# Performance work log

Measured on AMD Instinct MI355X. Metric: run time of the kernel, lower is better.

The kernel has to match this reference:

```python
import jax, jax.numpy as jnp
import numpy as np

N_NODES = 50000
N_EDGES = 300000
D = 256
EPS = 1e-12


def setup_inputs() -> dict:
    key = jax.random.key(0)
    ks = jax.random.split(key, 10)
    h5_all = jax.random.normal(ks[0], (N_NODES, D), dtype=jnp.float32)
    edge_index = jax.random.randint(ks[1], (2, N_EDGES), 0, N_NODES, dtype=jnp.int64)
    edge_weight = jax.random.uniform(ks[2], (N_EDGES,), dtype=jnp.float32)
    s = 1.0 / np.sqrt(D)
    W6 = jax.random.normal(ks[3], (D, D), dtype=jnp.float32) * s
    b6 = jnp.zeros((D,), dtype=jnp.float32)
    W7 = jax.random.normal(ks[4], (D, D), dtype=jnp.float32) * s
    b7 = jnp.zeros((D,), dtype=jnp.float32)
    Wp = jax.random.normal(ks[5], (D, D), dtype=jnp.float32) * s
    bp = jnp.zeros((D,), dtype=jnp.float32)
    return {"h5_all": h5_all, "edge_index": edge_index, "edge_weight": edge_weight,
            "W6": W6, "b6": b6, "W7": W7, "b7": b7, "Wp": Wp, "bp": bp}


def _gcn_layer(x, W, b, src, dst, norm, n_nodes):
    # x: [N, D]; transform then gather-scale-scatter along edges
    xt = x @ W                                   # [N, D]
    msg = xt[src] * norm[:, None]                # [E, D] gathered + scaled
    agg = jax.ops.segment_sum(msg, dst, num_segments=n_nodes)  # [N, D]
    return jax.nn.relu(agg + b)


def reference(h5_all, edge_index, edge_weight, W6, b6, W7, b7, Wp, bp):
    src, dst = edge_index[0], edge_index[1]
    # symmetric degree normalization with edge weights (GCN-style)
    deg_out = jax.ops.segment_sum(edge_weight, src, num_segments=N_NODES)
    deg_in = jax.ops.segment_sum(edge_weight, dst, num_segments=N_NODES)
    norm = edge_weight * jax.lax.rsqrt(deg_out[src] * deg_in[dst] + EPS)  # [E]
    h6 = _gcn_layer(h5_all, W6, b6, src, dst, norm, N_NODES)
    h7 = _gcn_layer(h6, W7, b7, src, dst, norm, N_NODES)
    out = h7 @ Wp + bp                           # post_mp linear head
    return out
```

## Files before the change

### kernel.cpp

```cpp
#include <hip/hip_runtime.h>

#define N_NODES 50000
#define N_PAD   50048
#define N_PANELS 3125
#define N_EDGES 300000
#define EPS_F 1e-12f
#define EB ((N_EDGES + 255) / 256)
#define GB 512
#define SCAN_NB ((N_NODES + 255) / 256)
#define MASK48 ((1ull << 48) - 1)
#define ZBYTES (N_NODES * 20)

typedef _Float16 f16x8 __attribute__((ext_vector_type(8)));
typedef float f32x4 __attribute__((ext_vector_type(4)));

static __device__ inline f32x4 mfma_f16(f16x8 a, f16x8 b, f32x4 c) {
    return __builtin_amdgcn_mfma_f32_16x16x32_f16(a, b, c, 0, 0, 0);
}

static __device__ inline size_t swz(int row, int l) {
    return ((size_t)(row >> 4) * 8 + (l >> 2)) * 512 + (size_t)((l & 3) * 128 + (row & 15) * 8);
}


__global__ __launch_bounds__(256) void zero_kernel(int4* __restrict__ p, int n16) {
    int i = blockIdx.x * 256 + threadIdx.x;
    if (i < n16) p[i] = make_int4(0, 0, 0, 0);
}


__global__ __launch_bounds__(256) void p1_kernel(const int* __restrict__ ei,
                                                 const float* __restrict__ ew,
                                                 unsigned long long* __restrict__ pk_out,
                                                 unsigned long long* __restrict__ pk_in,
                                                 const float* __restrict__ W6,
                                                 const float* __restrict__ W7,
                                                 const float* __restrict__ Wp,
                                                 _Float16* __restrict__ Bsw) {
    int b = blockIdx.x;
    if (b < EB) {
        int e = b * 256 + threadIdx.x;
        if (e >= N_EDGES) return;
        int s = ei[e];
        int d = ei[N_EDGES + e];
        unsigned long long wfx = (unsigned long long)(ew[e] * 4294967296.0f);
        atomicAdd(&pk_out[s], wfx);
        atomicAdd(&pk_in[d], (1ull << 48) | wfx);
    } else {
        int bb = b - EB;
        int wsel = bb >> 5;
        const float* W = (wsel == 0) ? W6 : (wsel == 1) ? W7 : Wp;
        int id = (bb & 31) * 256 + threadIdx.x;
        int n = id >> 5, l = id & 31;
        f16x8 o;
#pragma unroll
        for (int j = 0; j < 8; ++j)
            o[j] = (_Float16)W[(l * 8 + j) * 256 + n];
        *(f16x8*)&Bsw[(size_t)wsel * 65536 + swz(n, l)] = o;
    }
}


__global__ __launch_bounds__(256) void scan1_kernel(const unsigned long long* __restrict__ pk_in,
                                                    const unsigned long long* __restrict__ pk_out,
                                                    float* __restrict__ deg_in,
                                                    float* __restrict__ deg_out,
                                                    int* __restrict__ partial) {
    __shared__ int sh[256];
    int i = blockIdx.x * 256 + threadIdx.x;
    int c = 0;
    if (i < N_NODES) {
        unsigned long long p = pk_in[i];
        c = (int)(p >> 48);
        deg_in[i] = (float)(p & MASK48) * 0x1p-32f;
        deg_out[i] = (float)pk_out[i] * 0x1p-32f;
    }
    sh[threadIdx.x] = c;
    __syncthreads();
    for (int off = 128; off > 0; off >>= 1) {
        if (threadIdx.x < (unsigned)off) sh[threadIdx.x] += sh[threadIdx.x + off];
        __syncthreads();
    }
    if (threadIdx.x == 0) partial[blockIdx.x] = sh[0];
}

__global__ __launch_bounds__(256) void scan23_kernel(const unsigned long long* __restrict__ pk_in,
                                                     const int* __restrict__ partial,
                                                     int* __restrict__ row_ptr) {
    __shared__ int ps[256];
    __shared__ int sh[256];
    int t = threadIdx.x;
    int pv = (t < SCAN_NB) ? partial[t] : 0;
    ps[t] = pv;
    __syncthreads();
    for (int off = 1; off < 256; off <<= 1) {
        int x = (t >= off) ? ps[t - off] : 0;
        __syncthreads();
        ps[t] += x;
        __syncthreads();
    }
    int incl = ps[t];
    __syncthreads();
    ps[t] = incl - pv;
    __syncthreads();
    const int boff = ps[blockIdx.x];

    int i = blockIdx.x * 256 + t;
    int v = (i < N_NODES) ? (int)(pk_in[i] >> 48) : 0;
    sh[t] = v;
    __syncthreads();
    for (int off = 1; off < 256; off <<= 1) {
        int x = (t >= off) ? sh[t - off] : 0;
        __syncthreads();
        sh[t] += x;
        __syncthreads();
    }
    if (i < N_NODES) row_ptr[i] = sh[t] - v + boff;
    if (i == 0) row_ptr[N_NODES] = N_EDGES;
}


__global__ __launch_bounds__(256) void p2_kernel(const int* __restrict__ ei,
                                                 const float* __restrict__ ew,
                                                 const float* __restrict__ deg_out,
                                                 const float* __restrict__ deg_in,
                                                 const int* __restrict__ row_ptr,
                                                 int* __restrict__ cur,
                                                 int2* __restrict__ csr,
                                                 const float* __restrict__ h5,
                                                 const _Float16* __restrict__ Bsw,
                                                 _Float16* __restrict__ xt) {
    __shared__ _Float16 ebuf[4][16 * 72];

    if (blockIdx.x < EB) {
        int e = blockIdx.x * 256 + threadIdx.x;
        if (e >= N_EDGES) return;
        int s = ei[e];
        int d = ei[N_EDGES + e];
        float nm = ew[e] * rsqrtf(deg_out[s] * deg_in[d] + EPS_F);
        int pos = atomicAdd(&cur[d], 1);
        csr[row_ptr[d] + pos] = make_int2(s, __float_as_int(nm));
        return;
    }

    const int t = threadIdx.x;
    const int w = t >> 6, lane = t & 63;

    f16x8 bf[4][8];
#pragma unroll
    for (int cp4 = 0; cp4 < 4; ++cp4)
#pragma unroll
        for (int kb = 0; kb < 8; ++kb)
            bf[cp4][kb] = *(const f16x8*)&Bsw[(size_t)((w * 4 + cp4) * 8 + kb) * 512 + lane * 8];

    for (int p = blockIdx.x - EB; p < N_PANELS; p += GB) {
        const float* ab = &h5[(size_t)(p * 16 + (lane & 15)) * 256 + (lane >> 4) * 8];
        f16x8 af[8];
#pragma unroll
        for (int kb = 0; kb < 8; ++kb) {
            float4 v0 = *(const float4*)(ab + kb * 32);
            float4 v1 = *(const float4*)(ab + kb * 32 + 4);
            f16x8 a;
            a[0] = (_Float16)v0.x; a[1] = (_Float16)v0.y;
            a[2] = (_Float16)v0.z; a[3] = (_Float16)v0.w;
            a[4] = (_Float16)v1.x; a[5] = (_Float16)v1.y;
            a[6] = (_Float16)v1.z; a[7] = (_Float16)v1.w;
            af[kb] = a;
        }

        f32x4 acc[4];
#pragma unroll
        for (int cp4 = 0; cp4 < 4; ++cp4) acc[cp4] = (f32x4){0.f, 0.f, 0.f, 0.f};
#pragma unroll
        for (int kb = 0; kb < 8; ++kb)
#pragma unroll
            for (int cp4 = 0; cp4 < 4; ++cp4)
                acc[cp4] = mfma_f16(af[kb], bf[cp4][kb], acc[cp4]);

        _Float16* eb = ebuf[w];
        const int rq = 4 * (lane >> 4);
        const int lr = lane & 15;
#pragma unroll
        for (int cp4 = 0; cp4 < 4; ++cp4)
#pragma unroll
            for (int rr = 0; rr < 4; ++rr)
                eb[(rq + rr) * 72 + cp4 * 16 + lr] = (_Float16)acc[cp4][rr];
#pragma unroll
        for (int it = 0; it < 2; ++it) {
            int rl = it * 8 + (lane >> 3);
            f16x8 v = *(const f16x8*)&eb[rl * 72 + (lane & 7) * 8];
            *(f16x8*)&xt[(size_t)(p * 16 + rl) * 256 + w * 64 + (lane & 7) * 8] = v;
        }
    }
}


template <int MODE>
__global__ __launch_bounds__(256) void gemm_f16(const _Float16* __restrict__ Asw,
                                                const _Float16* __restrict__ Bsw,
                                                const float* __restrict__ bias,
                                                void* __restrict__ Cout) {
    __shared__ _Float16 ebuf[4][16 * 72];

    const int t = threadIdx.x;
    const int w = t >> 6, lane = t & 63;
    const int lr = lane & 15;

    f16x8 bf[4][8];
#pragma unroll
    for (int cp4 = 0; cp4 < 4; ++cp4)
#pragma unroll
        for (int kb = 0; kb < 8; ++kb)
            bf[cp4][kb] = *(const f16x8*)&Bsw[(size_t)((w * 4 + cp4) * 8 + kb) * 512 + lane * 8];

    float bc[4];
    if (MODE == 1) {
#pragma unroll
        for (int cp4 = 0; cp4 < 4; ++cp4) bc[cp4] = bias[w * 64 + cp4 * 16 + lr];
    }

    for (int p = blockIdx.x; p < N_PANELS; p += GB) {
        const _Float16* abase = &Asw[(size_t)p * 4096 + lane * 8];
        f16x8 af[8];
#pragma unroll
        for (int kb = 0; kb < 8; ++kb)
            af[kb] = *(const f16x8*)&abase[kb * 512];

        f32x4 acc[4];
#pragma unroll
        for (int cp4 = 0; cp4 < 4; ++cp4) acc[cp4] = (f32x4){0.f, 0.f, 0.f, 0.f};
#pragma unroll
        for (int kb = 0; kb < 8; ++kb)
#pragma unroll
            for (int cp4 = 0; cp4 < 4; ++cp4)
                acc[cp4] = mfma_f16(af[kb], bf[cp4][kb], acc[cp4]);

        if (MODE == 0) {
            _Float16* eb = ebuf[w];
            const int rq = 4 * (lane >> 4);
#pragma unroll
            for (int cp4 = 0; cp4 < 4; ++cp4)
#pragma unroll
                for (int rr = 0; rr < 4; ++rr)
                    eb[(rq + rr) * 72 + cp4 * 16 + lr] = (_Float16)acc[cp4][rr];
            _Float16* xp = (_Float16*)Cout;
#pragma unroll
            for (int it = 0; it < 2; ++it) {
                int rl = it * 8 + (lane >> 3);
                f16x8 v = *(const f16x8*)&eb[rl * 72 + (lane & 7) * 8];
                *(f16x8*)&xp[(size_t)(p * 16 + rl) * 256 + w * 64 + (lane & 7) * 8] = v;
            }
        } else {
            float* op = (float*)Cout;
            const int rbase = p * 16 + 4 * (lane >> 4);
#pragma unroll
            for (int cp4 = 0; cp4 < 4; ++cp4) {
                const int col = w * 64 + cp4 * 16 + lr;
#pragma unroll
                for (int rr = 0; rr < 4; ++rr)
                    op[(size_t)(rbase + rr) * 256 + col] = acc[cp4][rr] + bc[cp4];
            }
        }
    }
}


__global__ __launch_bounds__(256) void agg_kernel(const _Float16* __restrict__ xt,
                                                  const int* __restrict__ row_ptr,
                                                  const int2* __restrict__ csr,
                                                  const float* __restrict__ bias,
                                                  _Float16* __restrict__ Asw) {
    const int g = threadIdx.x >> 5;
    const int l = threadIdx.x & 31;
    const int v = blockIdx.x * 8 + g;
    const int d0 = l * 8;

    const int s0 = row_ptr[v];
    const int s1 = row_ptr[v + 1];

    float acc[8] = {0.f, 0.f, 0.f, 0.f, 0.f, 0.f, 0.f, 0.f};

    int i = s0;
    for (; i + 4 <= s1; i += 4) {
        int2 hd[4];
#pragma unroll
        for (int u = 0; u < 4; ++u) hd[u] = csr[i + u];
        f16x8 val[4];
#pragma unroll
        for (int u = 0; u < 4; ++u)
            val[u] = *(const f16x8*)&xt[(size_t)hd[u].x * 256 + d0];
#pragma unroll
        for (int u = 0; u < 4; ++u) {
            float wv = __int_as_float(hd[u].y);
#pragma unroll
            for (int j = 0; j < 8; ++j)
                acc[j] += (float)val[u][j] * wv;
        }
    }
    {
        int rem = s1 - i;
        int2 hd[3];
#pragma unroll
        for (int u = 0; u < 3; ++u)
            hd[u] = (u < rem) ? csr[i + u] : make_int2(0, 0);
        f16x8 val[3];
#pragma unroll
        for (int u = 0; u < 3; ++u)
            val[u] = *(const f16x8*)&xt[(size_t)hd[u].x * 256 + d0];
#pragma unroll
        for (int u = 0; u < 3; ++u) {
            float wv = __int_as_float(hd[u].y);
#pragma unroll
            for (int j = 0; j < 8; ++j)
                acc[j] += (float)val[u][j] * wv;
        }
    }

    f16x8 o;
#pragma unroll
    for (int j = 0; j < 8; ++j) {
        float r = acc[j] + bias[d0 + j];
        r = r > 0.f ? r : 0.f;
        o[j] = (_Float16)r;
    }
    *(f16x8*)&Asw[swz(v, l)] = o;
}


extern "C" void kernel_launch(void* const* d_in, const int* in_sizes, int n_in,
                              void* d_out, int out_size, void* d_ws, size_t ws_size,
                              hipStream_t stream) {
    (void)in_sizes; (void)n_in; (void)out_size; (void)ws_size;
    const float* h5 = (const float*)d_in[0];
    const int*   ei = (const int*)d_in[1];
    const float* ew = (const float*)d_in[2];
    const float* W6 = (const float*)d_in[3];
    const float* b6 = (const float*)d_in[4];
    const float* W7 = (const float*)d_in[5];
    const float* b7 = (const float*)d_in[6];
    const float* Wp = (const float*)d_in[7];
    const float* bp = (const float*)d_in[8];
    float* out = (float*)d_out;

    char* ws = (char*)d_ws;
    size_t off = 0;
    auto alloc = [&](size_t bytes) -> void* {
        void* p = ws + off;
        off = (off + bytes + 255) & ~(size_t)255;
        return p;
    };

    char* zblk = (char*)alloc(ZBYTES);
    unsigned long long* pk_out = (unsigned long long*)zblk;
    unsigned long long* pk_in  = (unsigned long long*)(zblk + N_NODES * 8);
    int* cur = (int*)(zblk + N_NODES * 16);

    float* deg_out = (float*)alloc(N_NODES * 4);
    float* deg_in  = (float*)alloc(N_NODES * 4);
    int*   row_ptr = (int*)alloc((N_NODES + 1) * 4);
    int*   partial = (int*)alloc(SCAN_NB * 4);
    int2*  csr     = (int2*)alloc(N_EDGES * 8);
    _Float16* Bsw  = (_Float16*)alloc(3 * 65536 * 2);
    _Float16* Asw  = (_Float16*)alloc((size_t)N_PAD * 256 * 2);
    _Float16* xt   = (_Float16*)alloc((size_t)N_PAD * 256 * 2);

    const int Z16 = ZBYTES / 16;

    zero_kernel<<<(Z16 + 255) / 256, 256, 0, stream>>>((int4*)zblk, Z16);

    p1_kernel<<<EB + 96, 256, 0, stream>>>(ei, ew, pk_out, pk_in, W6, W7, Wp, Bsw);
    scan1_kernel<<<SCAN_NB, 256, 0, stream>>>(pk_in, pk_out, deg_in, deg_out, partial);
    scan23_kernel<<<SCAN_NB, 256, 0, stream>>>(pk_in, partial, row_ptr);

    p2_kernel<<<EB + GB, 256, 0, stream>>>(ei, ew, deg_out, deg_in, row_ptr, cur, csr,
                                           h5, Bsw, xt);

    agg_kernel<<<N_NODES / 8, 256, 0, stream>>>(xt, row_ptr, csr, b6, Asw);
    gemm_f16<0><<<GB, 256, 0, stream>>>(Asw, Bsw + 65536, nullptr, xt);
    agg_kernel<<<N_NODES / 8, 256, 0, stream>>>(xt, row_ptr, csr, b7, Asw);
    gemm_f16<1><<<GB, 256, 0, stream>>>(Asw, Bsw + 2 * 65536, bp, out);
}
```

Before: 170.9 us.

## Pre-convert h5 to swizzled fp16 in p1 and stage final GEMM stores via LDS

The fp32-to-fp16 conversion of the input features moves out of the first GEMM and into extra blocks of the degree-counting kernel, which write a swizzled fp16 copy. The transform GEMM then loads pre-swizzled fp16 A tiles instead of strided fp32. This adds an extra full read and write of the features, exchanged for more coalesced A loads in the GEMM and overlap with the atomic-heavy edge pass. Separately, the final-output GEMM now stages results through shared memory so it can emit row-contiguous float4 stores instead of scattered scalar stores. Padding rows are dropped from the buffer allocations.

```diff
diff --git a/kernel.cpp b/kernel.cpp
--- a/kernel.cpp
+++ b/kernel.cpp
@@ -1,11 +1,12 @@
 #include <hip/hip_runtime.h>
 
 #define N_NODES 50000
-#define N_PAD   50048
 #define N_PANELS 3125
 #define N_EDGES 300000
 #define EPS_F 1e-12f
 #define EB ((N_EDGES + 255) / 256)
+#define WB 96
+#define AB (N_NODES * 32 / 256)
 #define GB 512
 #define SCAN_NB ((N_NODES + 255) / 256)
 #define MASK48 ((1ull << 48) - 1)
@@ -36,7 +37,9 @@
                                                  const float* __restrict__ W6,
                                                  const float* __restrict__ W7,
                                                  const float* __restrict__ Wp,
-                                                 _Float16* __restrict__ Bsw) {
+                                                 _Float16* __restrict__ Bsw,
+                                                 const float* __restrict__ h5,
+                                                 _Float16* __restrict__ Asw) {
     int b = blockIdx.x;
     if (b < EB) {
         int e = b * 256 + threadIdx.x;
@@ -46,7 +49,7 @@
         unsigned long long wfx = (unsigned long long)(ew[e] * 4294967296.0f);
         atomicAdd(&pk_out[s], wfx);
         atomicAdd(&pk_in[d], (1ull << 48) | wfx);
-    } else {
+    } else if (b < EB + WB) {
         int bb = b - EB;
         int wsel = bb >> 5;
         const float* W = (wsel == 0) ? W6 : (wsel == 1) ? W7 : Wp;
@@ -57,6 +60,18 @@
         for (int j = 0; j < 8; ++j)
             o[j] = (_Float16)W[(l * 8 + j) * 256 + n];
         *(f16x8*)&Bsw[(size_t)wsel * 65536 + swz(n, l)] = o;
+    } else {
+        int tid = (b - EB - WB) * 256 + threadIdx.x;
+        int row = tid >> 5, l = tid & 31;
+        const float* p = &h5[(size_t)row * 256 + l * 8];
+        float4 v0 = *(const float4*)p;
+        float4 v1 = *(const float4*)(p + 4);
+        f16x8 o;
+        o[0] = (_Float16)v0.x; o[1] = (_Float16)v0.y;
+        o[2] = (_Float16)v0.z; o[3] = (_Float16)v0.w;
+        o[4] = (_Float16)v1.x; o[5] = (_Float16)v1.y;
+        o[6] = (_Float16)v1.z; o[7] = (_Float16)v1.w;
+        *(f16x8*)&Asw[swz(row, l)] = o;
     }
 }
 
@@ -127,10 +142,10 @@
                                                  const int* __restrict__ row_ptr,
                                                  int* __restrict__ cur,
                                                  int2* __restrict__ csr,
-                                                 const float* __restrict__ h5,
+                                                 const _Float16* __restrict__ Asw,
                                                  const _Float16* __restrict__ Bsw,
                                                  _Float16* __restrict__ xt) {
-    __shared__ _Float16 ebuf[4][16 * 72];
+    __shared__ __align__(16) _Float16 ebuf[4][16 * 72];
 
     if (blockIdx.x < EB) {
         int e = blockIdx.x * 256 + threadIdx.x;
@@ -154,19 +169,11 @@
             bf[cp4][kb] = *(const f16x8*)&Bsw[(size_t)((w * 4 + cp4) * 8 + kb) * 512 + lane * 8];
 
     for (int p = blockIdx.x - EB; p < N_PANELS; p += GB) {
-        const float* ab = &h5[(size_t)(p * 16 + (lane & 15)) * 256 + (lane >> 4) * 8];
+        const _Float16* abase = &Asw[(size_t)p * 4096 + lane * 8];
         f16x8 af[8];
 #pragma unroll
-        for (int kb = 0; kb < 8; ++kb) {
-            float4 v0 = *(const float4*)(ab + kb * 32);
-            float4 v1 = *(const float4*)(ab + kb * 32 + 4);
-            f16x8 a;
-            a[0] = (_Float16)v0.x; a[1] = (_Float16)v0.y;
-            a[2] = (_Float16)v0.z; a[3] = (_Float16)v0.w;
-            a[4] = (_Float16)v1.x; a[5] = (_Float16)v1.y;
-            a[6] = (_Float16)v1.z; a[7] = (_Float16)v1.w;
-            af[kb] = a;
-        }
+        for (int kb = 0; kb < 8; ++kb)
+            af[kb] = *(const f16x8*)&abase[kb * 512];
 
         f32x4 acc[4];
 #pragma unroll
@@ -200,7 +207,7 @@
                                                 const _Float16* __restrict__ Bsw,
                                                 const float* __restrict__ bias,
                                                 void* __restrict__ Cout) {
-    __shared__ _Float16 ebuf[4][16 * 72];
+    __shared__ __align__(16) char ebraw[4][16 * 68 * 4];
 
     const int t = threadIdx.x;
     const int w = t >> 6, lane = t & 63;
@@ -235,9 +242,9 @@
             for (int cp4 = 0; cp4 < 4; ++cp4)
                 acc[cp4] = mfma_f16(af[kb], bf[cp4][kb], acc[cp4]);
 
+        const int rq = 4 * (lane >> 4);
         if (MODE == 0) {
-            _Float16* eb = ebuf[w];
-            const int rq = 4 * (lane >> 4);
+            _Float16* eb = (_Float16*)ebraw[w];
 #pragma unroll
             for (int cp4 = 0; cp4 < 4; ++cp4)
 #pragma unroll
@@ -251,14 +258,18 @@
                 *(f16x8*)&xp[(size_t)(p * 16 + rl) * 256 + w * 64 + (lane & 7) * 8] = v;
             }
         } else {
+            float* eb = (float*)ebraw[w];
+#pragma unroll
+            for (int cp4 = 0; cp4 < 4; ++cp4)
+#pragma unroll
+                for (int rr = 0; rr < 4; ++rr)
+                    eb[(rq + rr) * 68 + cp4 * 16 + lr] = acc[cp4][rr] + bc[cp4];
             float* op = (float*)Cout;
-            const int rbase = p * 16 + 4 * (lane >> 4);
-#pragma unroll
-            for (int cp4 = 0; cp4 < 4; ++cp4) {
-                const int col = w * 64 + cp4 * 16 + lr;
-#pragma unroll
-                for (int rr = 0; rr < 4; ++rr)
-                    op[(size_t)(rbase + rr) * 256 + col] = acc[cp4][rr] + bc[cp4];
+#pragma unroll
+            for (int it = 0; it < 4; ++it) {
+                int rl = it * 4 + (lane >> 4);
+                float4 v = *(const float4*)&eb[rl * 68 + lr * 4];
+                *(float4*)&op[(size_t)(p * 16 + rl) * 256 + w * 64 + lr * 4] = v;
             }
         }
     }
@@ -361,19 +372,21 @@
     int*   partial = (int*)alloc(SCAN_NB * 4);
     int2*  csr     = (int2*)alloc(N_EDGES * 8);
     _Float16* Bsw  = (_Float16*)alloc(3 * 65536 * 2);
-    _Float16* Asw  = (_Float16*)alloc((size_t)N_PAD * 256 * 2);
-    _Float16* xt   = (_Float16*)alloc((size_t)N_PAD * 256 * 2);
+    _Float16* Asw  = (_Float16*)alloc((size_t)N_NODES * 256 * 2);
+    _Float16* xt   = (_Float16*)alloc((size_t)N_NODES * 256 * 2);
 
     const int Z16 = ZBYTES / 16;
 
     zero_kernel<<<(Z16 + 255) / 256, 256, 0, stream>>>((int4*)zblk, Z16);
 
-    p1_kernel<<<EB + 96, 256, 0, stream>>>(ei, ew, pk_out, pk_in, W6, W7, Wp, Bsw);
+    p1_kernel<<<EB + WB + AB, 256, 0, stream>>>(ei, ew, pk_out, pk_in,
+                                                W6, W7, Wp, Bsw, h5, Asw);
+
     scan1_kernel<<<SCAN_NB, 256, 0, stream>>>(pk_in, pk_out, deg_in, deg_out, partial);
     scan23_kernel<<<SCAN_NB, 256, 0, stream>>>(pk_in, partial, row_ptr);
 
     p2_kernel<<<EB + GB, 256, 0, stream>>>(ei, ew, deg_out, deg_in, row_ptr, cur, csr,
-                                           h5, Bsw, xt);
+                                           Asw, Bsw, xt);
 
     agg_kernel<<<N_NODES / 8, 256, 0, stream>>>(xt, row_ptr, csr, b6, Asw);
     gemm_f16<0><<<GB, 256, 0, stream>>>(Asw, Bsw + 65536, nullptr, xt);
```

New measurement: 166.5 us. 2.5% less time.
